# Optimization experiments

Hardware: AMD Instinct MI355X
Metric: run time of the kernel (lower is better)

Reference implementation:

```python
import jax, jax.numpy as jnp
import numpy as np

D = 128      # memory_dim
L = 64       # segment_len
SCALE = 1.0 / np.sqrt(D)
LN_EPS = 1e-5


def _layernorm(x, g, b):
    mu = x.mean(-1, keepdims=True)
    var = ((x - mu) ** 2).mean(-1, keepdims=True)
    return (x - mu) * jax.lax.rsqrt(var + LN_EPS) * g + b


def setup_inputs() -> dict:
    key = jax.random.key(0)
    ks = jax.random.split(key, 8)
    B, T, Hd = 4, 4096, 2048
    w = 0.02  # init scale for weight matrices
    return {
        "H": jax.random.normal(ks[0], (B, T, Hd), jnp.float32),
        "M": jax.random.normal(ks[1], (B, D, D), jnp.float32),  # [B,K=128,D=128]
        "ln_g": jnp.ones((Hd,), jnp.float32),
        "ln_b": jnp.zeros((Hd,), jnp.float32),
        "W_eta_w": jax.random.normal(ks[2], (Hd,), jnp.float32) * w,
        "W_eta_b": jnp.full((1,), -5.0, jnp.float32),
        "sum_q": jax.random.normal(ks[3], (D,), jnp.float32),
        "sp_w": jax.random.normal(ks[4], (Hd, D), jnp.float32) * w,
        "sp_b": jnp.zeros((D,), jnp.float32),
        "eta_ch": jnp.ones((D,), jnp.float32),
        "temp": jnp.ones((1,), jnp.float32),
        "W_qkv": jax.random.normal(ks[5], (Hd, 3 * D), jnp.float32) * w,
    }


def reference(H, M, ln_g, ln_b, W_eta_w, W_eta_b, sum_q, sp_w, sp_b, eta_ch, temp, W_qkv):
    B, T, _ = H.shape
    K = M.shape[1]
    S = T // L  # T chosen divisible by segment_len (no-pad branch)

    Hn = _layernorm(H, ln_g, ln_b)                      # [B,T,Hd]

    # ---- write_memory ----
    H_mem = Hn @ sp_w + sp_b                            # [B,T,D]
    eta_tokens = jnp.einsum('bth,h->bt', Hn, W_eta_w) + W_eta_b  # [B,T]

    H_segs = H_mem.reshape(B, S, L, D)
    summary_scores = jnp.einsum('d,bsld->bsl', sum_q, H_segs) * SCALE
    summary_w = jax.nn.softmax(summary_scores, axis=-1)
    Z_seg = jnp.einsum('bsl,bsld->bsd', summary_w, H_segs)       # [B,S,D]

    eta_sig = jax.nn.sigmoid(eta_tokens)                          # [B,T]
    eta_seg = eta_sig.reshape(B, S, L).max(axis=-1)[..., None]    # [B,S,1]

    scores = jnp.einsum('bsd,bkd->bsk', Z_seg, M) * SCALE * jnp.exp(temp)
    A = jax.nn.softmax(scores, axis=-1)                           # [B,S,K]
    DeltaM = jnp.einsum('bsk,bsd->bkd', A, Z_seg * eta_seg)       # [B,K,D]

    eta_avg = eta_seg.mean(axis=1, keepdims=True)                 # [B,1,1]
    gate = eta_avg * jax.nn.sigmoid(eta_ch)                       # [B,1,D]
    M_new = (1.0 - gate) * M + DeltaM / S

    norm_sq = jnp.sum(DeltaM ** 2) / S
    # diversity loss on M_new
    Mn = M_new / jnp.maximum(jnp.linalg.norm(M_new, axis=-1, keepdims=True), 1e-12)
    sim = jnp.einsum('bkd,bjd->bkj', Mn, Mn) * (1.0 - jnp.eye(K, dtype=M.dtype))
    div_loss = jnp.mean(sim ** 2)
    loss = norm_sq * 0.01 + div_loss * 0.1

    # ---- read_memory (from updated memory; K<=1024 -> dense softmax path) ----
    Q_r = Hn @ W_qkv[:, 2 * D:]                                   # [B,T,D]
    r_scores = jnp.einsum('btd,bkd->btk', Q_r, M_new)
    A_r = jax.nn.softmax(r_scores * 2.0, axis=-1)
    C = jnp.einsum('btk,bkd->btd', A_r, M_new)                    # [B,T,D]

    return C, loss
```

## Files before the change

### kernel.cpp

```cpp
#include <hip/hip_runtime.h>
#include <hip/hip_bf16.h>
#include <math.h>

#define HD   2048
#define DD   128
#define TT   4096
#define BB   4
#define MT   (BB*TT)
#define LSEG 64
#define SSEG 64
#define NCOL 256
#define SCALE_D 0.088388347648318447f

typedef _Float16 half8 __attribute__((ext_vector_type(8)));
typedef _Float16 half4v __attribute__((ext_vector_type(4)));
typedef float    f32x4 __attribute__((ext_vector_type(4)));

__device__ __forceinline__ float sigmf(float x){ return 1.f/(1.f+__expf(-x)); }

__device__ __forceinline__ void glds16(const void* g, void* l) {
  __builtin_amdgcn_global_load_lds(
      (const __attribute__((address_space(1))) unsigned int*)g,
      (__attribute__((address_space(3))) unsigned int*)l, 16, 0, 0);
}

__global__ void k_pre(const float* __restrict__ ln_g, const float* __restrict__ ln_b,
                      const float* __restrict__ sp_w, const float* __restrict__ sp_b,
                      const float* __restrict__ W_qkv, const float* __restrict__ W_eta_w,
                      const float* __restrict__ W_eta_b,
                      _Float16* __restrict__ Bp, float* __restrict__ s_vec,
                      float* __restrict__ cb_vec, float* __restrict__ we2,
                      float* __restrict__ scal)
{
  __shared__ float red1[256], red2[256];
  int n = blockIdx.x, t = threadIdx.x;
  float sp = 0.f, cp = 0.f;
  if (n < NCOL) {
    for (int h = t; h < HD; h += 256) {
      float w = (n < DD) ? sp_w[(size_t)h*DD + n] : W_qkv[(size_t)h*384 + 256 + (n-DD)];
      float g = ln_g[h], b = ln_b[h];
      Bp[(size_t)n*HD + h] = (_Float16)(g*w);
      sp += g*w; cp += b*w;
    }
  } else {
    for (int h = t; h < HD; h += 256) {
      float w = W_eta_w[h];
      float g = ln_g[h], b = ln_b[h];
      we2[h] = g*w;
      sp += g*w; cp += b*w;
    }
  }
  red1[t] = sp; red2[t] = cp;
  __syncthreads();
  for (int o = 128; o > 0; o >>= 1) {
    if (t < o) { red1[t] += red1[t+o]; red2[t] += red2[t+o]; }
    __syncthreads();
  }
  if (t == 0) {
    if (n < NCOL) {
      s_vec[n]  = red1[0];
      cb_vec[n] = red2[0] + ((n < DD) ? sp_b[n] : 0.f);
    } else {
      scal[0] = red1[0];
      scal[1] = red2[0] + W_eta_b[0];
      scal[2] = 0.f; scal[3] = 0.f;
    }
  }
}

__launch_bounds__(512, 2)
__global__ void k01(const float* __restrict__ H, const _Float16* __restrict__ Bp,
                    const float* __restrict__ s_vec, const float* __restrict__ cb_vec,
                    const float* __restrict__ we2, const float* __restrict__ scal,
                    const float* __restrict__ sum_q, const float* __restrict__ Mmat,
                    const float* __restrict__ temp,
                    float* __restrict__ Q_r, float* __restrict__ Zeta,
                    float* __restrict__ A_seg, float* __restrict__ eta_seg)
{
  __shared__ __align__(16) char pool[147456];
  __shared__ float we_s[HD];
  __shared__ float smu[64], srs[64], seta[64];
  __shared__ float sq_s[128], w64_s[64], Zs[128], red_s[4];
  __shared__ float eta_sh_s;
  _Float16* sA  = (_Float16*)pool;
  _Float16* sB  = (_Float16*)(pool + 16384);
  float*    sHm = (float*)pool;

  int tid = threadIdx.x;
  int seg = blockIdx.x;
  int b   = seg >> 6;
  int m0  = seg * 64;
  int w = tid >> 6, lane = tid & 63;
  int wr = w >> 2, wc = w & 3;
  int fcol = lane & 15, kq = lane >> 4;

  for (int i = tid; i < HD/4; i += 512)
    ((float4*)we_s)[i] = ((const float4*)we2)[i];
  if (tid < 128) sq_s[tid] = sum_q[tid];
  float scal0 = scal[0], scal1 = scal[1];
  __syncthreads();

  int r_l = tid >> 3, s8 = tid & 7;
  const float* aptr = H + (size_t)(m0 + r_l)*HD + s8*8;
  int bn[4], bsl[4];
#pragma unroll
  for (int i = 0; i < 4; ++i) {
    int idx = i*512 + tid;
    bn[i]  = idx >> 3;
    bsl[i] = (idx & 7) ^ (bn[i] & 7);
  }

  f32x4 acc[2][4];
#pragma unroll
  for (int i = 0; i < 2; ++i)
#pragma unroll
    for (int j = 0; j < 4; ++j) acc[i][j] = (f32x4){0.f,0.f,0.f,0.f};
  float s1 = 0.f, s2 = 0.f, se = 0.f;

  float4 q0a = *(const float4*)(aptr + 0),   q0b = *(const float4*)(aptr + 4);
  float4 q1a = *(const float4*)(aptr + 64),  q1b = *(const float4*)(aptr + 68);
  __builtin_amdgcn_sched_barrier(0);
#pragma unroll
  for (int i = 0; i < 4; ++i)
    glds16(Bp + (size_t)bn[i]*HD + bsl[i]*8, sB + (size_t)(i*512 + tid)*8);
  __builtin_amdgcn_sched_barrier(0);
  float4 q2a = *(const float4*)(aptr + 128), q2b = *(const float4*)(aptr + 132);
  __builtin_amdgcn_sched_barrier(0);
#pragma unroll
  for (int i = 0; i < 4; ++i)
    glds16(Bp + (size_t)bn[i]*HD + 64 + bsl[i]*8,
           sB + 16384 + (size_t)(i*512 + tid)*8);
  __builtin_amdgcn_sched_barrier(0);
  float4 q3a = *(const float4*)(aptr + 192), q3b = *(const float4*)(aptr + 196);
  __builtin_amdgcn_sched_barrier(0);
#pragma unroll
  for (int i = 0; i < 4; ++i)
    glds16(Bp + (size_t)bn[i]*HD + 128 + bsl[i]*8,
           sB + 32768 + (size_t)(i*512 + tid)*8);
  __builtin_amdgcn_sched_barrier(0);

#define KSTEP(K0V, SAB, SBBUF, SBNB, P0, P1, VMASM, APREF, BISSUE)            \
  {                                                                           \
    _Float16* sAc = sA + (SAB)*4096;                                          \
    _Float16* sBc = sB + (SBBUF)*16384;                                       \
    const int k0 = (K0V);                                                     \
    {                                                                         \
      float v[8] = {P0.x,P0.y,P0.z,P0.w, P1.x,P1.y,P1.z,P1.w};                \
      const float4* wv4 = (const float4*)(we_s + k0 + s8*8);                  \
      float4 u0 = wv4[0], u1 = wv4[1];                                        \
      float uu[8] = {u0.x,u0.y,u0.z,u0.w, u1.x,u1.y,u1.z,u1.w};               \
      half8 h0;                                                               \
      _Pragma("unroll")                                                       \
      for (int j = 0; j < 8; ++j) {                                           \
        s1 += v[j]; s2 += v[j]*v[j]; se += v[j]*uu[j];                        \
        h0[j] = (_Float16)v[j];                                               \
      }                                                                       \
      *(half8*)&sAc[r_l*64 + (s8 ^ (r_l & 7))*8] = h0;                        \
    }                                                                         \
    asm volatile(VMASM ::: "memory");                                         \
    __builtin_amdgcn_s_barrier();                                             \
    __builtin_amdgcn_sched_barrier(0);                                        \
    if (BISSUE) {                                                             \
      _Float16* sBn = sB + (SBNB)*16384;                                      \
      const _Float16* bsrc = Bp + (k0 + 192);                                 \
      _Pragma("unroll")                                                       \
      for (int i = 0; i < 4; ++i)                                             \
        glds16(bsrc + (size_t)bn[i]*HD + bsl[i]*8,                            \
               sBn + (size_t)(i*512 + tid)*8);                                \
      __builtin_amdgcn_sched_barrier(0);                                      \
    }                                                                         \
    if (APREF) {                                                              \
      const float* ap_ = aptr + k0 + 256;                                     \
      P0 = *(const float4*)(ap_ + 0);                                         \
      P1 = *(const float4*)(ap_ + 4);                                         \
      __builtin_amdgcn_sched_barrier(0);                                      \
    }                                                                         \
    __builtin_amdgcn_s_setprio(1);                                            \
    _Pragma("unroll")                                                         \
    for (int ks = 0; ks < 2; ++ks) {                                          \
      half8 af[2], bf[4];                                                     \
      _Pragma("unroll")                                                       \
      for (int rt = 0; rt < 2; ++rt) {                                        \
        int r = wr*32 + rt*16 + fcol;                                         \
        int ch = (ks*4 + kq) ^ (r & 7);                                       \
        af[rt] = *(half8*)&sAc[r*64 + ch*8];                                  \
      }                                                                       \
      _Pragma("unroll")                                                       \
      for (int ct = 0; ct < 4; ++ct) {                                        \
        int n = wc*64 + ct*16 + fcol;                                         \
        int ch = (ks*4 + kq) ^ (n & 7);                                       \
        bf[ct] = *(half8*)&sBc[n*64 + ch*8];                                  \
      }                                                                       \
      _Pragma("unroll")                                                       \
      for (int rt = 0; rt < 2; ++rt)                                          \
        _Pragma("unroll")                                                     \
        for (int ct = 0; ct < 4; ++ct)                                        \
          acc[rt][ct] = __builtin_amdgcn_mfma_f32_16x16x32_f16(af[rt], bf[ct], acc[rt][ct], 0,0,0); \
    }                                                                         \
    __builtin_amdgcn_s_setprio(0);                                            \
  }

  KSTEP(0,   0, 0, 3, q0a, q0b, "s_waitcnt vmcnt(12) lgkmcnt(0)", 1, 1)
  KSTEP(64,  1, 1, 0, q1a, q1b, "s_waitcnt vmcnt(12) lgkmcnt(0)", 1, 1)
  KSTEP(128, 0, 2, 1, q2a, q2b, "s_waitcnt vmcnt(12) lgkmcnt(0)", 1, 1)
  KSTEP(192, 1, 3, 2, q3a, q3b, "s_waitcnt vmcnt(14) lgkmcnt(0)", 1, 1)
#pragma unroll 1
  for (int kp = 1; kp < 7; ++kp) {
    int j0 = kp*256;
    KSTEP(j0,     0, 0, 3, q0a, q0b, "s_waitcnt vmcnt(14) lgkmcnt(0)", 1, 1)
    KSTEP(j0+64,  1, 1, 0, q1a, q1b, "s_waitcnt vmcnt(14) lgkmcnt(0)", 1, 1)
    KSTEP(j0+128, 0, 2, 1, q2a, q2b, "s_waitcnt vmcnt(14) lgkmcnt(0)", 1, 1)
    KSTEP(j0+192, 1, 3, 2, q3a, q3b, "s_waitcnt vmcnt(14) lgkmcnt(0)", 1, 1)
  }
  KSTEP(1792, 0, 0, 3, q0a, q0b, "s_waitcnt vmcnt(14) lgkmcnt(0)", 0, 1)
  KSTEP(1856, 1, 1, 0, q1a, q1b, "s_waitcnt vmcnt(12) lgkmcnt(0)", 0, 0)
  KSTEP(1920, 0, 2, 1, q2a, q2b, "s_waitcnt vmcnt(6) lgkmcnt(0)",  0, 0)
  KSTEP(1984, 1, 3, 2, q3a, q3b, "s_waitcnt vmcnt(0) lgkmcnt(0)",  0, 0)
#undef KSTEP

  s1 += __shfl_xor(s1, 1); s1 += __shfl_xor(s1, 2); s1 += __shfl_xor(s1, 4);
  s2 += __shfl_xor(s2, 1); s2 += __shfl_xor(s2, 2); s2 += __shfl_xor(s2, 4);
  se += __shfl_xor(se, 1); se += __shfl_xor(se, 2); se += __shfl_xor(se, 4);
  if (s8 == 0) {
    float mu   = s1 * (1.f/HD);
    float var  = s2 * (1.f/HD) - mu*mu;
    float rstd = rsqrtf(var + 1e-5f);
    smu[r_l] = mu; srs[r_l] = rstd;
    seta[r_l] = rstd*(se - mu*scal0) + scal1;
  }
  __syncthreads();

#pragma unroll
  for (int ct = 0; ct < 4; ++ct) {
    int nl = wc*64 + ct*16 + fcol;
    float sn = s_vec[nl], cbn = cb_vec[nl];
#pragma unroll
    for (int rt = 0; rt < 2; ++rt)
#pragma unroll
      for (int r = 0; r < 4; ++r) {
        int m = wr*32 + rt*16 + kq*4 + r;
        sHm[m*260 + nl] = srs[m]*(acc[rt][ct][r] - smu[m]*sn) + cbn;
      }
  }
  __syncthreads();

#pragma unroll
  for (int j = 0; j < 4; ++j) {
    int idx = j*512 + tid;
    int row = idx >> 5, c4 = (idx & 31)*4;
    *(float4*)&Q_r[(size_t)(m0 + row)*DD + c4] = *(float4*)&sHm[row*260 + 128 + c4];
  }

  if (w == 0) {
    float sc = 0.f;
    const float4* hrow = (const float4*)&sHm[lane*260];
#pragma unroll
    for (int d4 = 0; d4 < 32; ++d4) {
      float4 hv = hrow[d4];
      float4 qv = *(const float4*)&sq_s[d4*4];
      sc += hv.x*qv.x + hv.y*qv.y + hv.z*qv.z + hv.w*qv.w;
    }
    sc *= SCALE_D;
    float mx = sc;
    for (int o = 32; o > 0; o >>= 1) mx = fmaxf(mx, __shfl_xor(mx, o));
    float e = __expf(sc - mx);
    float sm = e;
    for (int o = 32; o > 0; o >>= 1) sm += __shfl_xor(sm, o);
    w64_s[lane] = e / sm;
  } else if (w == 1) {
    float ev = seta[lane];
    for (int o = 32; o > 0; o >>= 1) ev = fmaxf(ev, __shfl_xor(ev, o));
    if (lane == 0) { float es = sigmf(ev); eta_sh_s = es; eta_seg[seg] = es; }
  }
  __syncthreads();

  if (tid < 128) {
    float z = 0.f;
    for (int l = 0; l < 64; ++l) z += w64_s[l]*sHm[l*260 + tid];
    Zs[tid] = z;
    Zeta[(size_t)seg*DD + tid] = z * eta_sh_s;
  }
  __syncthreads();

  float sc2 = 0.f;
  if (tid < 128) {
    const float4* mrow = (const float4*)(Mmat + ((size_t)b*DD + tid)*DD);
#pragma unroll
    for (int d4 = 0; d4 < 32; ++d4) {
      float4 mv = mrow[d4];
      sc2 += mv.x*Zs[d4*4] + mv.y*Zs[d4*4+1] + mv.z*Zs[d4*4+2] + mv.w*Zs[d4*4+3];
    }
    sc2 *= SCALE_D * __expf(temp[0]);
    float mx = sc2;
    for (int o = 32; o > 0; o >>= 1) mx = fmaxf(mx, __shfl_xor(mx, o));
    if (lane == 0) red_s[w] = mx;
  }
  __syncthreads();
  float ev2 = 0.f;
  if (tid < 128) {
    float mx = fmaxf(red_s[0], red_s[1]);
    ev2 = __expf(sc2 - mx);
    float sm = ev2;
    for (int o = 32; o > 0; o >>= 1) sm += __shfl_xor(sm, o);
    if (lane == 0) red_s[2 + w] = sm;
  }
  __syncthreads();
  if (tid < 128) {
    float smt = red_s[2] + red_s[3];
    A_seg[(size_t)seg*DD + tid] = ev2 / smt;
  }
}

__global__ void k2b(const float* __restrict__ A_seg, const float* __restrict__ Zeta,
                    const float* __restrict__ eta_seg, const float* __restrict__ Mmat,
                    const float* __restrict__ eta_ch,
                    float* __restrict__ M_new, float* __restrict__ rns_arr,
                    float* __restrict__ scal)
{
  __shared__ float As[64][33];
  __shared__ __align__(16) float Zsl[64*128];
  __shared__ float rowp[32][8];
  __shared__ float eta_av;
  __shared__ float redb[4];
  int tid = threadIdx.x;
  int b = blockIdx.x >> 2, kq = blockIdx.x & 3;
  for (int i = tid; i < 64*32; i += 256) {
    int s = i >> 5, j = i & 31;
    As[s][j] = A_seg[((size_t)b*SSEG + s)*DD + kq*32 + j];
  }
  const float4* z4 = (const float4*)(Zeta + (size_t)b*SSEG*DD);
  float4* zs4 = (float4*)Zsl;
  for (int i = tid; i < 64*32; i += 256) zs4[i] = z4[i];
  if (tid < 64) {
    float ev = eta_seg[(size_t)b*SSEG + tid];
    for (int o=32;o>0;o>>=1) ev += __shfl_xor(ev, o);
    if (tid == 0) eta_av = ev * (1.f/SSEG);
  }
  __syncthreads();
  int kl = tid & 31, dg = tid >> 5;
  int k = kq*32 + kl, d0 = dg*16;
  float dm[16];
#pragma unroll
  for (int j=0;j<16;j++) dm[j]=0.f;
  for (int s = 0; s < 64; ++s) {
    float a = As[s][kl];
    const float* zr = &Zsl[s*128 + d0];
#pragma unroll
    for (int j=0;j<16;j++) dm[j] += a * zr[j];
  }
  float nsq = 0.f;
#pragma unroll
  for (int j=0;j<16;j++) nsq += dm[j]*dm[j];
  float eav = eta_av;
  float mn[16];
  float ss = 0.f;
#pragma unroll
  for (int j=0;j<16;j++) {
    int d = d0 + j;
    float gate = eav * sigmf(eta_ch[d]);
    float v = (1.f - gate)*Mmat[((size_t)b*DD + k)*DD + d] + dm[j]*(1.f/SSEG);
    mn[j] = v; ss += v*v;
  }
#pragma unroll
  for (int j=0;j<16;j+=4) {
    float4 v4; v4.x=mn[j]; v4.y=mn[j+1]; v4.z=mn[j+2]; v4.w=mn[j+3];
    *(float4*)&M_new[((size_t)b*DD + k)*DD + d0 + j] = v4;
  }
  rowp[kl][dg] = ss;
  for (int o=1;o<64;o<<=1) nsq += __shfl_xor(nsq, o);
  if ((tid&63)==0) redb[tid>>6] = nsq;
  __syncthreads();
  if (tid == 0) atomicAdd(&scal[2], redb[0]+redb[1]+redb[2]+redb[3]);
  if (tid < 32) {
    float t2 = 0.f;
#pragma unroll
    for (int g=0; g<8; ++g) t2 += rowp[tid][g];
    float nrm = sqrtf(t2);
    rns_arr[(size_t)b*DD + kq*32 + tid] = 1.f / fmaxf(nrm, 1e-12f);
  }
}

__global__ void k2d(const float* __restrict__ M_new, const float* __restrict__ rns_arr,
                    float* __restrict__ scal)
{
  __shared__ float kr[4][128];
  __shared__ float redb[4];
  int tid = threadIdx.x;
  int b = blockIdx.x >> 5, kq = blockIdx.x & 31;
  for (int i = tid; i < 4*128; i += 256) {
    int ki = i >> 7, d = i & 127;
    kr[ki][d] = M_new[((size_t)b*DD + kq*4 + ki)*DD + d];
  }
  __syncthreads();
  int j = tid & 127, kh = tid >> 7;
  const float* mj = &M_new[((size_t)b*DD + j)*DD];
  float rj = rns_arr[(size_t)b*DD + j];
  float dv = 0.f;
#pragma unroll
  for (int ki2 = 0; ki2 < 2; ++ki2) {
    int kil = kh*2 + ki2;
    int kk = kq*4 + kil;
    float dot = 0.f;
    for (int d = 0; d < 128; d += 4) {
      float4 a = *(const float4*)(mj + d);
      dot += a.x*kr[kil][d] + a.y*kr[kil][d+1] + a.z*kr[kil][d+2] + a.w*kr[kil][d+3];
    }
    if (kk != j) {
      float sv = dot * rj * rns_arr[(size_t)b*DD + kk];
      dv += sv*sv;
    }
  }
  for (int o=1;o<64;o<<=1) dv += __shfl_xor(dv, o);
  if ((tid&63)==0) redb[tid>>6] = dv;
  __syncthreads();
  if (tid==0) atomicAdd(&scal[3], redb[0]+redb[1]+redb[2]+redb[3]);
}

__launch_bounds__(256, 1)
__global__ void k3(const float* __restrict__ Q_r, const float* __restrict__ M_new,
                   const float* __restrict__ scal, float* __restrict__ out)
{
  __shared__ __align__(16) _Float16 Mq[128*132];
  __shared__ __align__(16) _Float16 Mt[128*136];
  __shared__ __align__(16) _Float16 Ps[64*132];
  int tid = threadIdx.x;
  int b = blockIdx.x >> 6, tile = blockIdx.x & 63;
  int t0 = tile*64;
  if (blockIdx.x == 0 && tid == 0) {
    float loss = 0.01f*(scal[2]*(1.f/SSEG)) + 0.1f*(scal[3]*(1.f/(BB*DD*DD)));
    out[(size_t)MT*DD] = loss;
  }
  const float4* m4 = (const float4*)(M_new + (size_t)b*DD*DD);
#pragma unroll
  for (int it = 0; it < 4; ++it) {
    int sb = it*256 + tid;
    int rb = sb & 31, cb = sb >> 5;
    int r0 = rb*4, c0 = cb*4;
    float a[4][4];
#pragma unroll
    for (int j = 0; j < 4; ++j) {
      float4 v = m4[(size_t)(r0+j)*32 + cb];
      a[j][0]=v.x; a[j][1]=v.y; a[j][2]=v.z; a[j][3]=v.w;
    }
#pragma unroll
    for (int j = 0; j < 4; ++j) {
      half4v h; h.x=(_Float16)a[j][0]; h.y=(_Float16)a[j][1];
                h.z=(_Float16)a[j][2]; h.w=(_Float16)a[j][3];
      *(half4v*)&Mq[(r0+j)*132 + c0] = h;
    }
#pragma unroll
    for (int j2 = 0; j2 < 4; ++j2) {
      half4v h; h.x=(_Float16)a[0][j2]; h.y=(_Float16)a[1][j2];
                h.z=(_Float16)a[2][j2]; h.w=(_Float16)a[3][j2];
      *(half4v*)&Mt[(c0+j2)*136 + r0] = h;
    }
  }
  int w = tid >> 6, lane = tid & 63;
  int fcol = lane & 15, kq = lane >> 4;
  int tokA = t0 + w*16 + fcol;
  size_t qbase = ((size_t)b*TT + tokA)*DD;
  half8 af[4];
#pragma unroll
  for (int ks = 0; ks < 4; ++ks) {
    float4 q0 = *(const float4*)&Q_r[qbase + ks*32 + kq*8];
    float4 q1 = *(const float4*)&Q_r[qbase + ks*32 + kq*8 + 4];
    half8 h;
    h[0]=(_Float16)q0.x; h[1]=(_Float16)q0.y; h[2]=(_Float16)q0.z; h[3]=(_Float16)q0.w;
    h[4]=(_Float16)q1.x; h[5]=(_Float16)q1.y; h[6]=(_Float16)q1.z; h[7]=(_Float16)q1.w;
    af[ks] = h;
  }
  __syncthreads();
  f32x4 sacc[8];
#pragma unroll
  for (int nt = 0; nt < 8; ++nt) sacc[nt] = (f32x4){0.f,0.f,0.f,0.f};
#pragma unroll
  for (int nt = 0; nt < 8; ++nt)
#pragma unroll
    for (int ks = 0; ks < 4; ++ks) {
      half8 bf = *(half8*)&Mq[(nt*16 + fcol)*132 + ks*32 + kq*8];
      sacc[nt] = __builtin_amdgcn_mfma_f32_16x16x32_f16(af[ks], bf, sacc[nt], 0,0,0);
    }
#pragma unroll
  for (int nt = 0; nt < 8; ++nt)
#pragma unroll
    for (int r = 0; r < 4; ++r) sacc[nt][r] *= 2.f;
  float mx[4], sm[4];
#pragma unroll
  for (int r = 0; r < 4; ++r) {
    float m = sacc[0][r];
#pragma unroll
    for (int nt = 1; nt < 8; ++nt) m = fmaxf(m, sacc[nt][r]);
#pragma unroll
    for (int o = 1; o < 16; o <<= 1) m = fmaxf(m, __shfl_xor(m, o));
    mx[r] = m;
  }
#pragma unroll
  for (int r = 0; r < 4; ++r) sm[r] = 0.f;
#pragma unroll
  for (int nt = 0; nt < 8; ++nt)
#pragma unroll
    for (int r = 0; r < 4; ++r) {
      float e = __expf(sacc[nt][r] - mx[r]);
      sacc[nt][r] = e; sm[r] += e;
    }
#pragma unroll
  for (int r = 0; r < 4; ++r) {
    float s = sm[r];
#pragma unroll
    for (int o = 1; o < 16; o <<= 1) s += __shfl_xor(s, o);
    sm[r] = 1.f / s;
  }
#pragma unroll
  for (int nt = 0; nt < 8; ++nt)
#pragma unroll
    for (int r = 0; r < 4; ++r) {
      int tk = w*16 + kq*4 + r;
      Ps[tk*132 + nt*16 + fcol] = (_Float16)(sacc[nt][r]*sm[r]);
    }
  __syncthreads();
  half8 pf[4];
#pragma unroll
  for (int ks = 0; ks < 4; ++ks)
    pf[ks] = *(half8*)&Ps[(w*16 + fcol)*132 + ks*32 + kq*8];
  f32x4 cacc[8];
#pragma unroll
  for (int nt = 0; nt < 8; ++nt) cacc[nt] = (f32x4){0.f,0.f,0.f,0.f};
#pragma unroll
  for (int nt = 0; nt < 8; ++nt)
#pragma unroll
    for (int ks = 0; ks < 4; ++ks) {
      half8 bf = *(half8*)&Mt[(nt*16 + fcol)*136 + ks*32 + kq*8];
      cacc[nt] = __builtin_amdgcn_mfma_f32_16x16x32_f16(pf[ks], bf, cacc[nt], 0,0,0);
    }
#pragma unroll
  for (int nt = 0; nt < 8; ++nt)
#pragma unroll
    for (int r = 0; r < 4; ++r) {
      int tk = t0 + w*16 + kq*4 + r;
      out[((size_t)b*TT + tk)*DD + nt*16 + fcol] = cacc[nt][r];
    }
}

extern "C" void kernel_launch(void* const* d_in, const int* in_sizes, int n_in,
                              void* d_out, int out_size, void* d_ws, size_t ws_size,
                              hipStream_t stream)
{
  (void)in_sizes; (void)n_in; (void)out_size; (void)ws_size;
  const float* H       = (const float*)d_in[0];
  const float* Mmat    = (const float*)d_in[1];
  const float* ln_g    = (const float*)d_in[2];
  const float* ln_b    = (const float*)d_in[3];
  const float* W_eta_w = (const float*)d_in[4];
  const float* W_eta_b = (const float*)d_in[5];
  const float* sum_q   = (const float*)d_in[6];
  const float* sp_w    = (const float*)d_in[7];
  const float* sp_b    = (const float*)d_in[8];
  const float* eta_ch  = (const float*)d_in[9];
  const float* temp    = (const float*)d_in[10];
  const float* W_qkv   = (const float*)d_in[11];
  float* out           = (float*)d_out;

  char* wsb = (char*)d_ws;
  size_t off = 0;
  auto alloc = [&](size_t bytes) -> void* {
    void* p = wsb + off;
    off = (off + bytes + 255) & ~(size_t)255;
    return p;
  };
  _Float16* Bp   = (_Float16*)alloc((size_t)NCOL*HD*2);
  float* s_vec   = (float*)alloc(NCOL*4);
  float* cb_vec  = (float*)alloc(NCOL*4);
  float* we2     = (float*)alloc(HD*4);
  float* scal    = (float*)alloc(4*4);
  float* Q_r     = (float*)alloc((size_t)MT*DD*4);
  float* Zeta    = (float*)alloc((size_t)BB*SSEG*DD*4);
  float* A_seg   = (float*)alloc((size_t)BB*SSEG*DD*4);
  float* eta_seg = (float*)alloc((size_t)BB*SSEG*4);
  float* M_new   = (float*)alloc((size_t)BB*DD*DD*4);
  float* rns_arr = (float*)alloc((size_t)BB*DD*4);

  hipLaunchKernelGGL(k_pre, dim3(NCOL+1), dim3(256), 0, stream,
                     ln_g, ln_b, sp_w, sp_b, W_qkv, W_eta_w, W_eta_b,
                     Bp, s_vec, cb_vec, we2, scal);
  hipLaunchKernelGGL(k01, dim3(MT/64), dim3(512), 0, stream,
                     H, Bp, s_vec, cb_vec, we2, scal, sum_q, Mmat, temp,
                     Q_r, Zeta, A_seg, eta_seg);
  hipLaunchKernelGGL(k2b, dim3(16), dim3(256), 0, stream,
                     A_seg, Zeta, eta_seg, Mmat, eta_ch, M_new, rns_arr, scal);
  hipLaunchKernelGGL(k2d, dim3(128), dim3(256), 0, stream,
                     M_new, rns_arr, scal);
  hipLaunchKernelGGL(k3, dim3(256), dim3(256), 0, stream,
                     Q_r, M_new, scal, out);
}
```

Before: 89.00 us.

## Restructure k01 GEMM main loop into 3-stage B ring with interleaved staging

Reworks the fused LayerNorm+projection GEMM loop from a 4-buffer B prefetch ring to a 3-buffer ring, shrinking shared memory. Each 64-wide K step is split into two halves: B loads are issued between the first half's LDS reads and its MFMAs, and A fp32-to-fp16 staging plus the next A prefetch are interleaved into the second half, with the barrier moved to the end of each step. This is meant to hide the A conversion and global loads behind MFMA work and cut LDS use, but the shallower prefetch depth may expose more load latency.

```diff
diff --git a/kernel.cpp b/kernel.cpp
--- a/kernel.cpp
+++ b/kernel.cpp
@@ -77,7 +77,7 @@
                     float* __restrict__ Q_r, float* __restrict__ Zeta,
                     float* __restrict__ A_seg, float* __restrict__ eta_seg)
 {
-  __shared__ __align__(16) char pool[147456];
+  __shared__ __align__(16) char pool[114688];
   __shared__ float we_s[HD];
   __shared__ float smu[64], srs[64], seta[64];
   __shared__ float sq_s[128], w64_s[64], Zs[128], red_s[4];
@@ -117,105 +117,138 @@
     for (int j = 0; j < 4; ++j) acc[i][j] = (f32x4){0.f,0.f,0.f,0.f};
   float s1 = 0.f, s2 = 0.f, se = 0.f;
 
-  float4 q0a = *(const float4*)(aptr + 0),   q0b = *(const float4*)(aptr + 4);
-  float4 q1a = *(const float4*)(aptr + 64),  q1b = *(const float4*)(aptr + 68);
+  float4 t0 = *(const float4*)(aptr + 0);
+  float4 t1 = *(const float4*)(aptr + 4);
   __builtin_amdgcn_sched_barrier(0);
 #pragma unroll
   for (int i = 0; i < 4; ++i)
     glds16(Bp + (size_t)bn[i]*HD + bsl[i]*8, sB + (size_t)(i*512 + tid)*8);
   __builtin_amdgcn_sched_barrier(0);
-  float4 q2a = *(const float4*)(aptr + 128), q2b = *(const float4*)(aptr + 132);
+  float4 paE0 = *(const float4*)(aptr + 64),  paE1 = *(const float4*)(aptr + 68);
   __builtin_amdgcn_sched_barrier(0);
 #pragma unroll
   for (int i = 0; i < 4; ++i)
     glds16(Bp + (size_t)bn[i]*HD + 64 + bsl[i]*8,
            sB + 16384 + (size_t)(i*512 + tid)*8);
   __builtin_amdgcn_sched_barrier(0);
-  float4 q3a = *(const float4*)(aptr + 192), q3b = *(const float4*)(aptr + 196);
+  float4 paO0 = *(const float4*)(aptr + 128), paO1 = *(const float4*)(aptr + 132);
   __builtin_amdgcn_sched_barrier(0);
-#pragma unroll
-  for (int i = 0; i < 4; ++i)
-    glds16(Bp + (size_t)bn[i]*HD + 128 + bsl[i]*8,
-           sB + 32768 + (size_t)(i*512 + tid)*8);
+  {
+    float v[8] = {t0.x,t0.y,t0.z,t0.w, t1.x,t1.y,t1.z,t1.w};
+    const float4* wv4 = (const float4*)(we_s + s8*8);
+    float4 u0 = wv4[0], u1 = wv4[1];
+    float uu[8] = {u0.x,u0.y,u0.z,u0.w, u1.x,u1.y,u1.z,u1.w};
+    half8 h0;
+#pragma unroll
+    for (int jj = 0; jj < 8; ++jj) {
+      s1 += v[jj]; s2 += v[jj]*v[jj]; se += v[jj]*uu[jj];
+      h0[jj] = (_Float16)v[jj];
+    }
+    *(half8*)&sA[r_l*64 + (s8 ^ (r_l & 7))*8] = h0;
+  }
+  asm volatile("s_waitcnt vmcnt(8) lgkmcnt(0)" ::: "memory");
+  __builtin_amdgcn_s_barrier();
   __builtin_amdgcn_sched_barrier(0);
 
-#define KSTEP(K0V, SAB, SBBUF, SBNB, P0, P1, VMASM, APREF, BISSUE)            \
+#define KSTEP(K0V, SAB, CURB, WB, P0, P1, VMASM, STAGE, PAISS, BISS)          \
   {                                                                           \
     _Float16* sAc = sA + (SAB)*4096;                                          \
-    _Float16* sBc = sB + (SBBUF)*16384;                                       \
+    _Float16* sBc = sB + (CURB)*16384;                                        \
     const int k0 = (K0V);                                                     \
+                                                \
     {                                                                         \
-      float v[8] = {P0.x,P0.y,P0.z,P0.w, P1.x,P1.y,P1.z,P1.w};                \
-      const float4* wv4 = (const float4*)(we_s + k0 + s8*8);                  \
-      float4 u0 = wv4[0], u1 = wv4[1];                                        \
-      float uu[8] = {u0.x,u0.y,u0.z,u0.w, u1.x,u1.y,u1.z,u1.w};               \
-      half8 h0;                                                               \
-      _Pragma("unroll")                                                       \
-      for (int j = 0; j < 8; ++j) {                                           \
-        s1 += v[j]; s2 += v[j]*v[j]; se += v[j]*uu[j];                        \
-        h0[j] = (_Float16)v[j];                                               \
-      }                                                                       \
-      *(half8*)&sAc[r_l*64 + (s8 ^ (r_l & 7))*8] = h0;                        \
-    }                                                                         \
-    asm volatile(VMASM ::: "memory");                                         \
-    __builtin_amdgcn_s_barrier();                                             \
-    __builtin_amdgcn_sched_barrier(0);                                        \
-    if (BISSUE) {                                                             \
-      _Float16* sBn = sB + (SBNB)*16384;                                      \
-      const _Float16* bsrc = Bp + (k0 + 192);                                 \
-      _Pragma("unroll")                                                       \
-      for (int i = 0; i < 4; ++i)                                             \
-        glds16(bsrc + (size_t)bn[i]*HD + bsl[i]*8,                            \
-               sBn + (size_t)(i*512 + tid)*8);                                \
-      __builtin_amdgcn_sched_barrier(0);                                      \
-    }                                                                         \
-    if (APREF) {                                                              \
-      const float* ap_ = aptr + k0 + 256;                                     \
-      P0 = *(const float4*)(ap_ + 0);                                         \
-      P1 = *(const float4*)(ap_ + 4);                                         \
-      __builtin_amdgcn_sched_barrier(0);                                      \
-    }                                                                         \
-    __builtin_amdgcn_s_setprio(1);                                            \
-    _Pragma("unroll")                                                         \
-    for (int ks = 0; ks < 2; ++ks) {                                          \
       half8 af[2], bf[4];                                                     \
       _Pragma("unroll")                                                       \
       for (int rt = 0; rt < 2; ++rt) {                                        \
         int r = wr*32 + rt*16 + fcol;                                         \
-        int ch = (ks*4 + kq) ^ (r & 7);                                       \
-        af[rt] = *(half8*)&sAc[r*64 + ch*8];                                  \
+        af[rt] = *(half8*)&sAc[r*64 + (kq ^ (r & 7))*8];                      \
       }                                                                       \
       _Pragma("unroll")                                                       \
       for (int ct = 0; ct < 4; ++ct) {                                        \
         int n = wc*64 + ct*16 + fcol;                                         \
-        int ch = (ks*4 + kq) ^ (n & 7);                                       \
-        bf[ct] = *(half8*)&sBc[n*64 + ch*8];                                  \
+        bf[ct] = *(half8*)&sBc[n*64 + (kq ^ (n & 7))*8];                      \
       }                                                                       \
+      if (BISS) {                                                             \
+        _Float16* sBn = sB + (WB)*16384;                                      \
+        const _Float16* bsrc = Bp + (k0 + 128);                               \
+        _Pragma("unroll")                                                     \
+        for (int i = 0; i < 4; ++i)                                           \
+          glds16(bsrc + (size_t)bn[i]*HD + bsl[i]*8,                          \
+                 sBn + (size_t)(i*512 + tid)*8);                              \
+      }                                                                       \
+      __builtin_amdgcn_sched_barrier(0);                                      \
+      __builtin_amdgcn_s_setprio(1);                                          \
       _Pragma("unroll")                                                       \
       for (int rt = 0; rt < 2; ++rt)                                          \
         _Pragma("unroll")                                                     \
         for (int ct = 0; ct < 4; ++ct)                                        \
           acc[rt][ct] = __builtin_amdgcn_mfma_f32_16x16x32_f16(af[rt], bf[ct], acc[rt][ct], 0,0,0); \
+      __builtin_amdgcn_s_setprio(0);                                          \
+      __builtin_amdgcn_sched_barrier(0);                                      \
     }                                                                         \
-    __builtin_amdgcn_s_setprio(0);                                            \
-  }
-
-  KSTEP(0,   0, 0, 3, q0a, q0b, "s_waitcnt vmcnt(12) lgkmcnt(0)", 1, 1)
-  KSTEP(64,  1, 1, 0, q1a, q1b, "s_waitcnt vmcnt(12) lgkmcnt(0)", 1, 1)
-  KSTEP(128, 0, 2, 1, q2a, q2b, "s_waitcnt vmcnt(12) lgkmcnt(0)", 1, 1)
-  KSTEP(192, 1, 3, 2, q3a, q3b, "s_waitcnt vmcnt(14) lgkmcnt(0)", 1, 1)
+                                 \
+    {                                                                         \
+      half8 af[2], bf[4];                                                     \
+      _Pragma("unroll")                                                       \
+      for (int rt = 0; rt < 2; ++rt) {                                        \
+        int r = wr*32 + rt*16 + fcol;                                         \
+        af[rt] = *(half8*)&sAc[r*64 + ((4 + kq) ^ (r & 7))*8];                \
+      }                                                                       \
+      _Pragma("unroll")                                                       \
+      for (int ct = 0; ct < 4; ++ct) {                                        \
+        int n = wc*64 + ct*16 + fcol;                                         \
+        bf[ct] = *(half8*)&sBc[n*64 + ((4 + kq) ^ (n & 7))*8];                \
+      }                                                                       \
+      __builtin_amdgcn_sched_barrier(0);                                      \
+      if (STAGE) {                                                            \
+        float v[8] = {P0.x,P0.y,P0.z,P0.w, P1.x,P1.y,P1.z,P1.w};              \
+        const float4* wv4 = (const float4*)(we_s + k0 + 64 + s8*8);           \
+        float4 u0 = wv4[0], u1 = wv4[1];                                      \
+        float uu[8] = {u0.x,u0.y,u0.z,u0.w, u1.x,u1.y,u1.z,u1.w};             \
+        half8 h0;                                                             \
+        _Pragma("unroll")                                                     \
+        for (int jj = 0; jj < 8; ++jj) {                                      \
+          s1 += v[jj]; s2 += v[jj]*v[jj]; se += v[jj]*uu[jj];                 \
+          h0[jj] = (_Float16)v[jj];                                           \
+        }                                                                     \
+        *(half8*)&sA[((SAB)^1)*4096 + r_l*64 + (s8 ^ (r_l & 7))*8] = h0;      \
+      }                                                                       \
+      if (PAISS) {                                                            \
+        P0 = *(const float4*)(aptr + k0 + 192);                               \
+        P1 = *(const float4*)(aptr + k0 + 196);                               \
+      }                                                                       \
+      __builtin_amdgcn_sched_barrier(0);                                      \
+      __builtin_amdgcn_s_setprio(1);                                          \
+      _Pragma("unroll")                                                       \
+      for (int rt = 0; rt < 2; ++rt)                                          \
+        _Pragma("unroll")                                                     \
+        for (int ct = 0; ct < 4; ++ct)                                        \
+          acc[rt][ct] = __builtin_amdgcn_mfma_f32_16x16x32_f16(af[rt], bf[ct], acc[rt][ct], 0,0,0); \
+      __builtin_amdgcn_s_setprio(0);                                          \
+      asm volatile(VMASM " lgkmcnt(0)" ::: "memory");                         \
+      __builtin_amdgcn_s_barrier();                                           \
+      __builtin_amdgcn_sched_barrier(0);                                      \
+    }                                                                         \
+  }
+
 #pragma unroll 1
-  for (int kp = 1; kp < 7; ++kp) {
-    int j0 = kp*256;
-    KSTEP(j0,     0, 0, 3, q0a, q0b, "s_waitcnt vmcnt(14) lgkmcnt(0)", 1, 1)
-    KSTEP(j0+64,  1, 1, 0, q1a, q1b, "s_waitcnt vmcnt(14) lgkmcnt(0)", 1, 1)
-    KSTEP(j0+128, 0, 2, 1, q2a, q2b, "s_waitcnt vmcnt(14) lgkmcnt(0)", 1, 1)
-    KSTEP(j0+192, 1, 3, 2, q3a, q3b, "s_waitcnt vmcnt(14) lgkmcnt(0)", 1, 1)
-  }
-  KSTEP(1792, 0, 0, 3, q0a, q0b, "s_waitcnt vmcnt(14) lgkmcnt(0)", 0, 1)
-  KSTEP(1856, 1, 1, 0, q1a, q1b, "s_waitcnt vmcnt(12) lgkmcnt(0)", 0, 0)
-  KSTEP(1920, 0, 2, 1, q2a, q2b, "s_waitcnt vmcnt(6) lgkmcnt(0)",  0, 0)
-  KSTEP(1984, 1, 3, 2, q3a, q3b, "s_waitcnt vmcnt(0) lgkmcnt(0)",  0, 0)
+  for (int kp = 0; kp < 4; ++kp) {
+    int j0 = kp*384;
+    KSTEP(j0,       0, 0, 2, paE0, paE1, "s_waitcnt vmcnt(8)", 1, 1, 1)
+    KSTEP(j0 + 64,  1, 1, 0, paO0, paO1, "s_waitcnt vmcnt(8)", 1, 1, 1)
+    KSTEP(j0 + 128, 0, 2, 1, paE0, paE1, "s_waitcnt vmcnt(8)", 1, 1, 1)
+    KSTEP(j0 + 192, 1, 0, 2, paO0, paO1, "s_waitcnt vmcnt(8)", 1, 1, 1)
+    KSTEP(j0 + 256, 0, 1, 0, paE0, paE1, "s_waitcnt vmcnt(8)", 1, 1, 1)
+    KSTEP(j0 + 320, 1, 2, 1, paO0, paO1, "s_waitcnt vmcnt(8)", 1, 1, 1)
+  }
+  KSTEP(1536, 0, 0, 2, paE0, paE1, "s_waitcnt vmcnt(8)", 1, 1, 1)
+  KSTEP(1600, 1, 1, 0, paO0, paO1, "s_waitcnt vmcnt(8)", 1, 1, 1)
+  KSTEP(1664, 0, 2, 1, paE0, paE1, "s_waitcnt vmcnt(8)", 1, 1, 1)
+  KSTEP(1728, 1, 0, 2, paO0, paO1, "s_waitcnt vmcnt(8)", 1, 1, 1)
+  KSTEP(1792, 0, 1, 0, paE0, paE1, "s_waitcnt vmcnt(8)", 1, 1, 1)
+  KSTEP(1856, 1, 2, 1, paO0, paO1, "s_waitcnt vmcnt(6)", 1, 0, 1)
+  KSTEP(1920, 0, 0, 2, paE0, paE1, "s_waitcnt vmcnt(0)", 1, 0, 0)
+  KSTEP(1984, 1, 1, 0, paO0, paO1, "s_waitcnt vmcnt(0)", 0, 0, 0)
 #undef KSTEP
 
   s1 += __shfl_xor(s1, 1); s1 += __shfl_xor(s1, 2); s1 += __shfl_xor(s1, 4);
```

New measurement: 88.35 us. About the same (-0.7%).
